# Kernel optimization log

Hardware: AMD Instinct MI355X
Metric: run time of the kernel (lower is better)

The kernel has to match this reference:

```python
import jax, jax.numpy as jnp
import numpy as np

EPS = 1e-5  # torch LayerNorm default


def setup_inputs() -> dict:
    key = jax.random.key(0)
    ks = jax.random.split(key, 4)
    B, S, D = 8, 1024, 768
    return {
        "q": jax.random.normal(ks[0], (B, S, D), dtype=jnp.float32),
        "k": jax.random.normal(ks[1], (B, S, D), dtype=jnp.float32),
        "v": jax.random.normal(ks[2], (B, S, D), dtype=jnp.float32),
        "W": jax.random.normal(ks[3], (D, D), dtype=jnp.float32) * (1.0 / np.sqrt(D)),
        "gamma": jnp.ones((D,), dtype=jnp.float32),
        "beta": jnp.zeros((D,), dtype=jnp.float32),
        "n_heads": 12,
    }


def reference(q, k, v, W, gamma, beta, n_heads):
    # Shapes: q,k,v [B,S,D]; W [D,D] (torch Linear weight, y = x @ W.T)
    B, S, D = q.shape
    Dh = D // n_heads

    proj = lambda x: jax.nn.relu(x @ W.T)
    q1, k1, v1 = proj(q), proj(k), proj(v)

    # chunk(dim=2) + cat(dim=0) == reshape to per-head [B,S,H,Dh]
    split = lambda x: x.reshape(B, S, n_heads, Dh)
    qh, kh, vh = split(q1), split(k1), split(v1)

    scale = 1.0 / (Dh ** 0.5)
    scores = jnp.einsum("bqhd,bkhd->bhqk", qh, kh) * scale  # [B,H,S,S]
    attn = jax.nn.softmax(scores, axis=-1)  # dropout is identity in eval mode
    out = jnp.einsum("bhqk,bkhd->bqhd", attn, vh).reshape(B, S, D)

    # `outputs += outputs + q` in torch -> outputs = 2*outputs + q
    out = 2.0 * out + q

    mu = jnp.mean(out, axis=-1, keepdims=True)
    var = jnp.var(out, axis=-1, keepdims=True)
    return (out - mu) / jnp.sqrt(var + EPS) * gamma + beta
```

## Files before the change

### kernel.cpp

```cpp
#include <hip/hip_runtime.h>
#include <hip/hip_bf16.h>

#define B_  8
#define S_  1024
#define D_  768
#define H_  12
#define DH_ 64

typedef __attribute__((ext_vector_type(8))) short bf16x8;
typedef __attribute__((ext_vector_type(4))) float f32x4;
typedef __attribute__((ext_vector_type(16))) float f32x16;

__device__ inline short f2bf(float f) {
    unsigned u = __builtin_bit_cast(unsigned, f);
    u = (u + 0x7fffu + ((u >> 16) & 1u)) >> 16;
    return (short)u;
}
__device__ inline float exp2_fast(float x) {
    float r; asm("v_exp_f32 %0, %1" : "=v"(r) : "v"(x)); return r;
}
__device__ inline unsigned cvt_pk_bf16(float lo, float hi) {
    unsigned r; asm("v_cvt_pk_bf16_f32 %0, %1, %2" : "=v"(r) : "v"(lo), "v"(hi)); return r;
}
__device__ inline float rcp_fast(float x) {
    float r; asm("v_rcp_f32 %0, %1" : "=v"(r) : "v"(x)); return r;
}
__device__ inline void plswap(unsigned& a, unsigned& b) {
    auto r = __builtin_amdgcn_permlane32_swap(a, b, false, false);
    a = r[0]; b = r[1];
}
__device__ inline float2 xhalves(float x) {
    unsigned u = __builtin_bit_cast(unsigned, x);
    auto r = __builtin_amdgcn_permlane32_swap(u, u, false, false);
    return make_float2(__builtin_bit_cast(float, r[0]),
                       __builtin_bit_cast(float, r[1]));
}
__device__ inline void gl_lds16(const float* gsrc, char* ldst) {
    __builtin_amdgcn_global_load_lds(
        (const __attribute__((address_space(1))) unsigned int*)gsrc,
        (__attribute__((address_space(3))) unsigned int*)ldst,
        16, 0, 0);
}

__global__ __launch_bounds__(256) void proj_kernel(
    const float* __restrict__ q, const float* __restrict__ k,
    const float* __restrict__ v, const float* __restrict__ W,
    short* __restrict__ q1, short* __restrict__ k1, short* __restrict__ v1t)
{
    __shared__ __align__(16) char lds_raw[32768];

    int p  = blockIdx.x;
    int L  = (p & 7) * 144 + (p >> 3);
    int mt = L / 6, nt = L % 6;
    int t  = mt >> 6;
    int m0 = (mt & 63) << 7;
    int n0 = nt << 7;
    const float* X = (t == 0) ? q : (t == 1) ? k : v;

    int tid = threadIdx.x, lane = tid & 63, w = tid >> 6;
    int wr = w >> 1, wc = w & 1;
    int l15 = lane & 15, g = lane >> 4;

    const float* srcA[4];
    const float* srcB[4];
    #pragma unroll
    for (int i = 0; i < 4; i++) {
        int r  = w * 32 + i * 8 + (lane >> 3);
        int sp = (lane & 7) ^ (r & 7);
        srcA[i] = X + (size_t)(m0 + r) * D_ + sp * 4;
        srcB[i] = W + (size_t)(n0 + r) * D_ + sp * 4;
    }

    f32x4 acc[4][4];
    #pragma unroll
    for (int m = 0; m < 4; m++)
        #pragma unroll
        for (int n = 0; n < 4; n++) acc[m][n] = (f32x4){0.f, 0.f, 0.f, 0.f};

    for (int kb = 0; kb < 24; ++kb) {
        __builtin_amdgcn_s_barrier();
        asm volatile("" ::: "memory");
        #pragma unroll
        for (int i = 0; i < 4; i++) {
            gl_lds16(srcA[i] + kb * 32, lds_raw + w * 4096 + i * 1024);
            gl_lds16(srcB[i] + kb * 32, lds_raw + 16384 + w * 4096 + i * 1024);
        }
        asm volatile("s_waitcnt vmcnt(0)" ::: "memory");
        __builtin_amdgcn_s_barrier();
        asm volatile("" ::: "memory");

        bf16x8 af[4], bfv[4];
        #pragma unroll
        for (int m = 0; m < 4; m++) {
            int r = wr * 64 + m * 16 + l15;
            const char* rp = lds_raw + r * 128;
            f32x4 lo = *(const f32x4*)(rp + (((2 * g)     ^ (r & 7)) << 4));
            f32x4 hi = *(const f32x4*)(rp + (((2 * g + 1) ^ (r & 7)) << 4));
            uint4 pk;
            pk.x = cvt_pk_bf16(lo[0], lo[1]); pk.y = cvt_pk_bf16(lo[2], lo[3]);
            pk.z = cvt_pk_bf16(hi[0], hi[1]); pk.w = cvt_pk_bf16(hi[2], hi[3]);
            af[m] = __builtin_bit_cast(bf16x8, pk);
        }
        #pragma unroll
        for (int n = 0; n < 4; n++) {
            int r = wc * 64 + n * 16 + l15;
            const char* rp = lds_raw + 16384 + r * 128;
            f32x4 lo = *(const f32x4*)(rp + (((2 * g)     ^ (r & 7)) << 4));
            f32x4 hi = *(const f32x4*)(rp + (((2 * g + 1) ^ (r & 7)) << 4));
            uint4 pk;
            pk.x = cvt_pk_bf16(lo[0], lo[1]); pk.y = cvt_pk_bf16(lo[2], lo[3]);
            pk.z = cvt_pk_bf16(hi[0], hi[1]); pk.w = cvt_pk_bf16(hi[2], hi[3]);
            bfv[n] = __builtin_bit_cast(bf16x8, pk);
        }
        __builtin_amdgcn_s_setprio(1);
        #pragma unroll
        for (int m = 0; m < 4; m++)
            #pragma unroll
            for (int n = 0; n < 4; n++)
                acc[m][n] = __builtin_amdgcn_mfma_f32_16x16x32_bf16(
                    af[m], bfv[n], acc[m][n], 0, 0, 0);
        __builtin_amdgcn_s_setprio(0);
    }

    __syncthreads();
    const float sc1 = (t == 1) ? 0.18033688011112793f : 1.0f;
    #pragma unroll
    for (int m = 0; m < 4; m++) {
        int rb = wr * 64 + m * 16 + (g << 2);
        #pragma unroll
        for (int n = 0; n < 4; n++) {
            int cb = wc * 64 + n * 16 + l15;
            #pragma unroll
            for (int r = 0; r < 4; r++) {
                short vv = f2bf(fmaxf(acc[m][n][r], 0.f) * sc1);
                int rr = (t == 2) ? cb : rb + r;
                int cc = (t == 2) ? rb + r : cb;
                *(short*)(lds_raw + rr * 256 + (((cc >> 3) ^ (rr & 15)) << 4)
                          + ((cc & 7) << 1)) = vv;
            }
        }
    }
    __syncthreads();
    int row = tid >> 1;
    int c0  = (tid & 1) << 6;
    bf16x8 ov[8];
    #pragma unroll
    for (int j = 0; j < 8; j++)
        ov[j] = *(const bf16x8*)(lds_raw + row * 256 +
                 ((((c0 >> 3) + j) ^ (row & 15)) << 4));
    if (t == 2) {
        int gc = n0 + row;
        int hh2 = gc >> 6, dh = gc & 63;
        int bb = m0 >> 10, s0 = m0 & 1023;
        short* dst = v1t + (((size_t)bb * H_ + hh2) * DH_ + dh) * S_ + s0 + c0;
        #pragma unroll
        for (int j = 0; j < 8; j++) *(bf16x8*)(dst + j * 8) = ov[j];
    } else {
        int m = m0 + row;
        int bb = m >> 10, ss = m & 1023;
        int hh2 = (n0 >> 6) + (tid & 1);
        short* dst = (t ? k1 : q1) + (((size_t)bb * H_ + hh2) * S_ + ss) * DH_;
        #pragma unroll
        for (int j = 0; j < 8; j++) *(bf16x8*)(dst + j * 8) = ov[j];
    }
}

__global__ __launch_bounds__(256, 3) void attn_kernel(
    const short* __restrict__ q1, const short* __restrict__ k1,
    const short* __restrict__ v1t, float* __restrict__ out)
{
    __shared__ short Klds[2][4096];
    __shared__ short Vlds[2][4096];
    __shared__ float lsum_lds[4][32];

    int d    = blockIdx.x;
    int head = (d & 7) + ((d >> 6) << 3);
    int qi   = (d >> 3) & 7;
    int bb   = head / H_, hh = head % H_;

    int tid = threadIdx.x, lane = tid & 63, w = tid >> 6;
    int l31 = lane & 31, hi = lane >> 5;
    int qbase = (qi * 4 + w) * 32;

    const short* Qp = q1  + (size_t)head * S_ * DH_;
    const short* Kp = k1  + (size_t)head * S_ * DH_;
    const short* Vp = v1t + (size_t)head * DH_ * S_;

    int sr = tid >> 2, sc = tid & 3;
    int swz0 = sr * 128 + ((sc       ^ (sr & 7)) << 4);
    int swz1 = sr * 128 + (((sc + 4) ^ (sr & 7)) << 4);

    bf16x8 stK0, stK1, stV0, stV1;

#define LOADST(kvb) do { \
        const short* _kg = Kp + (size_t)((kvb) + sr) * DH_; \
        const short* _vg = Vp + (size_t)sr * S_ + (kvb); \
        stK0 = *(const bf16x8*)(_kg + sc * 8); \
        stK1 = *(const bf16x8*)(_kg + (sc + 4) * 8); \
        stV0 = *(const bf16x8*)(_vg + sc * 8); \
        stV1 = *(const bf16x8*)(_vg + (sc + 4) * 8); \
    } while (0)
#define WRITEST(buf) do { \
        char* _kb = (char*)&Klds[buf][0]; \
        char* _vb = (char*)&Vlds[buf][0]; \
        *(bf16x8*)(_kb + swz0) = stK0; \
        *(bf16x8*)(_kb + swz1) = stK1; \
        *(bf16x8*)(_vb + swz0) = stV0; \
        *(bf16x8*)(_vb + swz1) = stV1; \
    } while (0)

    bf16x8 qf[4];
    #pragma unroll
    for (int kb = 0; kb < 4; kb++)
        qf[kb] = *(const bf16x8*)(Qp + (size_t)(qbase + l31) * DH_ + kb * 16 + hi * 8);

    f32x16 o0, o1;
    #pragma unroll
    for (int r = 0; r < 16; r++) { o0[r] = 0.f; o1[r] = 0.f; }
    float mreg = -1e30f, lsum = 0.f;

    int xk = l31 & 7;

    auto subtile = [&](int cur, int j) {
        const char* Kt = (const char*)&Klds[cur][0];
        const char* Vt = (const char*)&Vlds[cur][0];
        int rK = (32 * j + l31) * 128;
        bf16x8 kf0 = *(const bf16x8*)(Kt + rK + (((0 + hi) ^ xk) << 4));
        bf16x8 kf1 = *(const bf16x8*)(Kt + rK + (((2 + hi) ^ xk) << 4));
        bf16x8 kf2 = *(const bf16x8*)(Kt + rK + (((4 + hi) ^ xk) << 4));
        bf16x8 kf3 = *(const bf16x8*)(Kt + rK + (((6 + hi) ^ xk) << 4));
        int rV0 = l31 * 128, rV1 = (32 + l31) * 128;
        int s0 = ((4 * j + hi) ^ xk) << 4, s1 = ((4 * j + 2 + hi) ^ xk) << 4;
        bf16x8 vf00 = *(const bf16x8*)(Vt + rV0 + s0);
        bf16x8 vf01 = *(const bf16x8*)(Vt + rV0 + s1);
        bf16x8 vf10 = *(const bf16x8*)(Vt + rV1 + s0);
        bf16x8 vf11 = *(const bf16x8*)(Vt + rV1 + s1);

        f32x16 s;
        #pragma unroll
        for (int r = 0; r < 16; r++) s[r] = 0.f;
        __builtin_amdgcn_s_setprio(1);
        s = __builtin_amdgcn_mfma_f32_32x32x16_bf16(kf0, qf[0], s, 0, 0, 0);
        s = __builtin_amdgcn_mfma_f32_32x32x16_bf16(kf1, qf[1], s, 0, 0, 0);
        s = __builtin_amdgcn_mfma_f32_32x32x16_bf16(kf2, qf[2], s, 0, 0, 0);
        s = __builtin_amdgcn_mfma_f32_32x32x16_bf16(kf3, qf[3], s, 0, 0, 0);
        __builtin_amdgcn_s_setprio(0);

        float t0 = fmaxf(s[0], s[1]),   t1 = fmaxf(s[2], s[3]);
        float t2 = fmaxf(s[4], s[5]),   t3 = fmaxf(s[6], s[7]);
        float t4 = fmaxf(s[8], s[9]),   t5 = fmaxf(s[10], s[11]);
        float t6 = fmaxf(s[12], s[13]), t7 = fmaxf(s[14], s[15]);
        float u0 = fmaxf(t0, t1), u1 = fmaxf(t2, t3);
        float u2 = fmaxf(t4, t5), u3 = fmaxf(t6, t7);
        float pmax = fmaxf(fmaxf(u0, u1), fmaxf(u2, u3));
        float2 ph = xhalves(pmax);
        pmax = fmaxf(ph.x, ph.y);

        if (!__all(pmax <= mreg + 8.f)) {
            float mn = fmaxf(mreg, pmax);
            float sc_ = exp2_fast(mreg - mn);
            mreg = mn; lsum *= sc_;
            if (hi == 0) lsum_lds[w][l31] = sc_;
            asm volatile("s_waitcnt lgkmcnt(0)" ::: "memory");
            #pragma unroll
            for (int r = 0; r < 16; r++) {
                int crow = (r & 3) + ((r >> 2) << 3) + (hi << 2);
                float srw = lsum_lds[w][crow];
                o0[r] *= srw; o1[r] *= srw;
            }
        }

        #pragma unroll
        for (int r = 0; r < 16; r++) s[r] = exp2_fast(s[r] - mreg);

        float a0 = s[0] + s[1],   a1 = s[2] + s[3];
        float a2 = s[4] + s[5],   a3 = s[6] + s[7];
        float a4 = s[8] + s[9],   a5 = s[10] + s[11];
        float a6 = s[12] + s[13], a7 = s[14] + s[15];
        float rsum = ((a0 + a1) + (a2 + a3)) + ((a4 + a5) + (a6 + a7));
        float2 rh = xhalves(rsum);
        lsum += rh.x + rh.y;

        unsigned c0 = cvt_pk_bf16(s[0], s[1]);
        unsigned c1 = cvt_pk_bf16(s[2], s[3]);
        unsigned c2 = cvt_pk_bf16(s[4], s[5]);
        unsigned c3 = cvt_pk_bf16(s[6], s[7]);
        unsigned c4 = cvt_pk_bf16(s[8], s[9]);
        unsigned c5 = cvt_pk_bf16(s[10], s[11]);
        unsigned c6 = cvt_pk_bf16(s[12], s[13]);
        unsigned c7 = cvt_pk_bf16(s[14], s[15]);
        plswap(c0, c2);
        plswap(c1, c3);
        plswap(c4, c6);
        plswap(c5, c7);

        union U { unsigned u[4]; bf16x8 v; };
        U f0, f1;
        f0.u[0] = c0; f0.u[1] = c1; f0.u[2] = c2; f0.u[3] = c3;
        f1.u[0] = c4; f1.u[1] = c5; f1.u[2] = c6; f1.u[3] = c7;

        __builtin_amdgcn_s_setprio(1);
        o0 = __builtin_amdgcn_mfma_f32_32x32x16_bf16(f0.v, vf00, o0, 0, 0, 0);
        o0 = __builtin_amdgcn_mfma_f32_32x32x16_bf16(f1.v, vf01, o0, 0, 0, 0);
        o1 = __builtin_amdgcn_mfma_f32_32x32x16_bf16(f0.v, vf10, o1, 0, 0, 0);
        o1 = __builtin_amdgcn_mfma_f32_32x32x16_bf16(f1.v, vf11, o1, 0, 0, 0);
        __builtin_amdgcn_s_setprio(0);
    };

    LOADST(0);
    WRITEST(0);
    LOADST(64);
    asm volatile("s_waitcnt lgkmcnt(0)" ::: "memory");
    __builtin_amdgcn_s_barrier();
    asm volatile("" ::: "memory");

    int cur = 0;
    for (int t = 0; t < 16; t++) {
        if (t < 15) {
            WRITEST(cur ^ 1);
            if (t < 14) LOADST((t + 2) * 64);
        }
        subtile(cur, 0);
        subtile(cur, 1);
        if (t < 15) {
            asm volatile("" ::: "memory");
            asm volatile("s_waitcnt lgkmcnt(0)" ::: "memory");
            __builtin_amdgcn_s_barrier();
            asm volatile("" ::: "memory");
        }
        cur ^= 1;
    }
#undef LOADST
#undef WRITEST

    if (hi == 0) lsum_lds[w][l31] = lsum;
    asm volatile("s_waitcnt lgkmcnt(0)" ::: "memory");
    #pragma unroll
    for (int r = 0; r < 16; r++) {
        int crow = (r & 3) + ((r >> 2) << 3) + (hi << 2);
        float inv = rcp_fast(lsum_lds[w][crow]);
        float* op = out + ((size_t)(bb * S_ + qbase + crow)) * D_ + hh * DH_ + l31;
        op[0]  = o0[r] * inv;
        op[32] = o1[r] * inv;
    }
}

__global__ __launch_bounds__(192) void ln_kernel(
    const float* __restrict__ qin, const float* __restrict__ gamma,
    const float* __restrict__ beta, float* __restrict__ out)
{
    int row = blockIdx.x;
    int tid = threadIdx.x;
    size_t base = (size_t)row * D_ + tid * 4;

    f32x4 o  = *(const f32x4*)(out + base);
    f32x4 qv = *(const f32x4*)(qin + base);
    f32x4 x;
    float sum = 0.f, sq = 0.f;
    #pragma unroll
    for (int i = 0; i < 4; i++) {
        x[i] = 2.f * o[i] + qv[i];
        sum += x[i];
        sq  += x[i] * x[i];
    }
    #pragma unroll
    for (int msk = 1; msk < 64; msk <<= 1) {
        sum += __shfl_xor(sum, msk);
        sq  += __shfl_xor(sq, msk);
    }
    __shared__ float s1[3], s2[3];
    if ((tid & 63) == 0) { s1[tid >> 6] = sum; s2[tid >> 6] = sq; }
    __syncthreads();
    sum = s1[0] + s1[1] + s1[2];
    sq  = s2[0] + s2[1] + s2[2];
    float mu   = sum * (1.f / D_);
    float var  = sq * (1.f / D_) - mu * mu;
    float rstd = rsqrtf(var + 1e-5f);
    f32x4 g = *(const f32x4*)(gamma + tid * 4);
    f32x4 b = *(const f32x4*)(beta + tid * 4);
    f32x4 y;
    #pragma unroll
    for (int i = 0; i < 4; i++)
        y[i] = (x[i] - mu) * rstd * g[i] + b[i];
    *(f32x4*)(out + base) = y;
}

extern "C" void kernel_launch(void* const* d_in, const int* in_sizes, int n_in,
                              void* d_out, int out_size, void* d_ws, size_t ws_size,
                              hipStream_t stream)
{
    const float* q     = (const float*)d_in[0];
    const float* k     = (const float*)d_in[1];
    const float* v     = (const float*)d_in[2];
    const float* W     = (const float*)d_in[3];
    const float* gamma = (const float*)d_in[4];
    const float* beta  = (const float*)d_in[5];

    size_t per = (size_t)B_ * H_ * S_ * DH_;
    short* q1  = (short*)d_ws;
    short* k1  = q1 + per;
    short* v1t = k1 + per;
    float* out = (float*)d_out;

    proj_kernel<<<dim3(1152), dim3(256), 0, stream>>>(q, k, v, W, q1, k1, v1t);
    attn_kernel<<<dim3(768), dim3(256), 0, stream>>>(q1, k1, v1t, out);
    ln_kernel<<<dim3(B_ * S_), dim3(192), 0, stream>>>(q, gamma, beta, out);
}
```

Measured before the change: 128.0 us.

## Pre-convert W to bf16 and retile projection GEMM with double-buffered loads

Adds a small kernel that converts W to bf16 once per call, so the projection GEMM loads half the weight bytes and skips per-tile conversion of B operands. The projection kernel moves to 512 threads with 64x384 tiles, where each wave owns 48 output columns, and the LDS loads become double-buffered so the next k-slice is fetched during compute. The epilogue is rewritten for the new tile shape. The cost is an extra kernel launch, a larger LDS footprint (64KB) and a workspace buffer for Wb.

Result: faster. 117.5 us, median of 2 (-8.2%).

```diff
diff --git a/kernel.cpp b/kernel.cpp
--- a/kernel.cpp
+++ b/kernel.cpp
@@ -35,65 +35,86 @@
     return make_float2(__builtin_bit_cast(float, r[0]),
                        __builtin_bit_cast(float, r[1]));
 }
-__device__ inline void gl_lds16(const float* gsrc, char* ldst) {
+__device__ inline void gl_lds16(const void* gsrc, char* ldst) {
     __builtin_amdgcn_global_load_lds(
         (const __attribute__((address_space(1))) unsigned int*)gsrc,
         (__attribute__((address_space(3))) unsigned int*)ldst,
         16, 0, 0);
 }
 
-__global__ __launch_bounds__(256) void proj_kernel(
+__global__ __launch_bounds__(256) void convw_kernel(
+    const float* __restrict__ W, short* __restrict__ Wb)
+{
+    int i = (blockIdx.x * 256 + threadIdx.x) * 8;
+    f32x4 a = *(const f32x4*)(W + i);
+    f32x4 b = *(const f32x4*)(W + i + 4);
+    uint4 pk;
+    pk.x = cvt_pk_bf16(a[0], a[1]); pk.y = cvt_pk_bf16(a[2], a[3]);
+    pk.z = cvt_pk_bf16(b[0], b[1]); pk.w = cvt_pk_bf16(b[2], b[3]);
+    *(uint4*)(Wb + i) = pk;
+}
+
+__global__ __launch_bounds__(512) void proj_kernel(
     const float* __restrict__ q, const float* __restrict__ k,
-    const float* __restrict__ v, const float* __restrict__ W,
+    const float* __restrict__ v, const short* __restrict__ Wb,
     short* __restrict__ q1, short* __restrict__ k1, short* __restrict__ v1t)
 {
-    __shared__ __align__(16) char lds_raw[32768];
+    __shared__ __align__(16) char lds[65536];
 
     int p  = blockIdx.x;
-    int L  = (p & 7) * 144 + (p >> 3);
-    int mt = L / 6, nt = L % 6;
-    int t  = mt >> 6;
-    int m0 = (mt & 63) << 7;
-    int n0 = nt << 7;
+    int L  = (p & 7) * 96 + (p >> 3);
+    int mt = L >> 1, nb = L & 1;
+    int t  = mt >> 7;
+    int m0 = (mt & 127) << 6;
+    int n0 = nb * 384;
     const float* X = (t == 0) ? q : (t == 1) ? k : v;
 
     int tid = threadIdx.x, lane = tid & 63, w = tid >> 6;
-    int wr = w >> 1, wc = w & 1;
     int l15 = lane & 15, g = lane >> 4;
 
-    const float* srcA[4];
-    const float* srcB[4];
-    #pragma unroll
-    for (int i = 0; i < 4; i++) {
-        int r  = w * 32 + i * 8 + (lane >> 3);
-        int sp = (lane & 7) ^ (r & 7);
-        srcA[i] = X + (size_t)(m0 + r) * D_ + sp * 4;
-        srcB[i] = W + (size_t)(n0 + r) * D_ + sp * 4;
-    }
-
-    f32x4 acc[4][4];
+    int xrow = w * 8 + (lane >> 3), xc = lane & 7;
+    const float* xsrc = X + (size_t)(m0 + xrow) * D_ + ((xc ^ (xrow & 7)) << 2);
+    char* xdst = lds + w * 1024;
+    int wrow0 = w * 48 + (lane >> 2), wc = lane & 3;
+    int wrow1 = wrow0 + 16, wrow2 = wrow0 + 32;
+    const short* wsrc0 = Wb + (size_t)(n0 + wrow0) * D_ + ((wc ^ ((wrow0 >> 1) & 3)) << 3);
+    const short* wsrc1 = Wb + (size_t)(n0 + wrow1) * D_ + ((wc ^ ((wrow1 >> 1) & 3)) << 3);
+    const short* wsrc2 = Wb + (size_t)(n0 + wrow2) * D_ + ((wc ^ ((wrow2 >> 1) & 3)) << 3);
+    char* wdst = lds + 16384 + w * 3072;
+
+#define ISSUE(s_, b_) do { int _ko = (s_) * 32; \
+        gl_lds16(xsrc + _ko, xdst + (b_) * 8192); \
+        gl_lds16(wsrc0 + _ko, wdst + (b_) * 24576); \
+        gl_lds16(wsrc1 + _ko, wdst + (b_) * 24576 + 1024); \
+        gl_lds16(wsrc2 + _ko, wdst + (b_) * 24576 + 2048); \
+    } while (0)
+
+    f32x4 acc[4][3];
     #pragma unroll
     for (int m = 0; m < 4; m++)
         #pragma unroll
-        for (int n = 0; n < 4; n++) acc[m][n] = (f32x4){0.f, 0.f, 0.f, 0.f};
-
-    for (int kb = 0; kb < 24; ++kb) {
+        for (int n = 0; n < 3; n++) acc[m][n] = (f32x4){0.f, 0.f, 0.f, 0.f};
+
+    ISSUE(0, 0);
+    for (int s = 0; s < 24; ++s) {
         __builtin_amdgcn_s_barrier();
         asm volatile("" ::: "memory");
-        #pragma unroll
-        for (int i = 0; i < 4; i++) {
-            gl_lds16(srcA[i] + kb * 32, lds_raw + w * 4096 + i * 1024);
-            gl_lds16(srcB[i] + kb * 32, lds_raw + 16384 + w * 4096 + i * 1024);
-        }
-        asm volatile("s_waitcnt vmcnt(0)" ::: "memory");
+        if (s + 1 < 24) {
+            ISSUE(s + 1, (s + 1) & 1);
+            asm volatile("s_waitcnt vmcnt(4)" ::: "memory");
+        } else {
+            asm volatile("s_waitcnt vmcnt(0)" ::: "memory");
+        }
         __builtin_amdgcn_s_barrier();
         asm volatile("" ::: "memory");
 
-        bf16x8 af[4], bfv[4];
+        const char* Xb = lds + (s & 1) * 8192;
+        const char* Wp = lds + 16384 + (s & 1) * 24576;
+        bf16x8 af[4];
         #pragma unroll
         for (int m = 0; m < 4; m++) {
-            int r = wr * 64 + m * 16 + l15;
-            const char* rp = lds_raw + r * 128;
+            int r = m * 16 + l15;
+            const char* rp = Xb + r * 128;
             f32x4 lo = *(const f32x4*)(rp + (((2 * g)     ^ (r & 7)) << 4));
             f32x4 hi = *(const f32x4*)(rp + (((2 * g + 1) ^ (r & 7)) << 4));
             uint4 pk;
@@ -101,67 +122,64 @@
             pk.z = cvt_pk_bf16(hi[0], hi[1]); pk.w = cvt_pk_bf16(hi[2], hi[3]);
             af[m] = __builtin_bit_cast(bf16x8, pk);
         }
-        #pragma unroll
-        for (int n = 0; n < 4; n++) {
-            int r = wc * 64 + n * 16 + l15;
-            const char* rp = lds_raw + 16384 + r * 128;
-            f32x4 lo = *(const f32x4*)(rp + (((2 * g)     ^ (r & 7)) << 4));
-            f32x4 hi = *(const f32x4*)(rp + (((2 * g + 1) ^ (r & 7)) << 4));
-            uint4 pk;
-            pk.x = cvt_pk_bf16(lo[0], lo[1]); pk.y = cvt_pk_bf16(lo[2], lo[3]);
-            pk.z = cvt_pk_bf16(hi[0], hi[1]); pk.w = cvt_pk_bf16(hi[2], hi[3]);
-            bfv[n] = __builtin_bit_cast(bf16x8, pk);
+        bf16x8 bfv[3];
+        #pragma unroll
+        for (int n = 0; n < 3; n++) {
+            int r = w * 48 + n * 16 + l15;
+            bfv[n] = *(const bf16x8*)(Wp + r * 64 + ((g ^ ((r >> 1) & 3)) << 4));
         }
         __builtin_amdgcn_s_setprio(1);
         #pragma unroll
         for (int m = 0; m < 4; m++)
             #pragma unroll
-            for (int n = 0; n < 4; n++)
+            for (int n = 0; n < 3; n++)
                 acc[m][n] = __builtin_amdgcn_mfma_f32_16x16x32_bf16(
                     af[m], bfv[n], acc[m][n], 0, 0, 0);
         __builtin_amdgcn_s_setprio(0);
     }
+#undef ISSUE
 
     __syncthreads();
     const float sc1 = (t == 1) ? 0.18033688011112793f : 1.0f;
     #pragma unroll
-    for (int m = 0; m < 4; m++) {
-        int rb = wr * 64 + m * 16 + (g << 2);
-        #pragma unroll
-        for (int n = 0; n < 4; n++) {
-            int cb = wc * 64 + n * 16 + l15;
+    for (int m = 0; m < 4; m++)
+        #pragma unroll
+        for (int n = 0; n < 3; n++)
             #pragma unroll
             for (int r = 0; r < 4; r++) {
+                int row = m * 16 + g * 4 + r;
+                int col = w * 48 + n * 16 + l15;
                 short vv = f2bf(fmaxf(acc[m][n][r], 0.f) * sc1);
-                int rr = (t == 2) ? cb : rb + r;
-                int cc = (t == 2) ? rb + r : cb;
-                *(short*)(lds_raw + rr * 256 + (((cc >> 3) ^ (rr & 15)) << 4)
-                          + ((cc & 7) << 1)) = vv;
+                if (t == 2)
+                    *(short*)(lds + col * 128 + (((row >> 3) ^ (col & 7)) << 4)
+                              + ((row & 7) << 1)) = vv;
+                else
+                    *(short*)(lds + row * 768 + (((col >> 3) ^ (row & 7)) << 4)
+                              + ((col & 7) << 1)) = vv;
             }
-        }
-    }
     __syncthreads();
-    int row = tid >> 1;
-    int c0  = (tid & 1) << 6;
-    bf16x8 ov[8];
-    #pragma unroll
-    for (int j = 0; j < 8; j++)
-        ov[j] = *(const bf16x8*)(lds_raw + row * 256 +
-                 ((((c0 >> 3) + j) ^ (row & 15)) << 4));
+    int bb2 = m0 >> 10;
     if (t == 2) {
-        int gc = n0 + row;
-        int hh2 = gc >> 6, dh = gc & 63;
-        int bb = m0 >> 10, s0 = m0 & 1023;
-        short* dst = v1t + (((size_t)bb * H_ + hh2) * DH_ + dh) * S_ + s0 + c0;
-        #pragma unroll
-        for (int j = 0; j < 8; j++) *(bf16x8*)(dst + j * 8) = ov[j];
+        #pragma unroll
+        for (int j = 0; j < 6; j++) {
+            int c = tid * 6 + j;
+            int vr = c >> 3, ch = c & 7;
+            bf16x8 val = *(const bf16x8*)(lds + vr * 128 + ((ch ^ (vr & 7)) << 4));
+            int gc = n0 + vr, h = gc >> 6, dh = gc & 63;
+            *(bf16x8*)(v1t + (((size_t)bb2 * H_ + h) * DH_ + dh) * S_
+                       + (m0 & 1023) + ch * 8) = val;
+        }
     } else {
-        int m = m0 + row;
-        int bb = m >> 10, ss = m & 1023;
-        int hh2 = (n0 >> 6) + (tid & 1);
-        short* dst = (t ? k1 : q1) + (((size_t)bb * H_ + hh2) * S_ + ss) * DH_;
-        #pragma unroll
-        for (int j = 0; j < 8; j++) *(bf16x8*)(dst + j * 8) = ov[j];
+        short* dst0 = t ? k1 : q1;
+        #pragma unroll
+        for (int j = 0; j < 6; j++) {
+            int c = tid * 6 + j;
+            int row = c / 48, ch = c % 48;
+            bf16x8 val = *(const bf16x8*)(lds + row * 768 + ((ch ^ (row & 7)) << 4));
+            int m = m0 + row, ss = m & 1023;
+            int gc = n0 + ch * 8, h = gc >> 6, dh = gc & 63;
+            *(bf16x8*)(dst0 + (((size_t)bb2 * H_ + h) * S_ + ss) * DH_ + dh) = val;
+        }
     }
 }
 
@@ -400,9 +418,11 @@
     short* q1  = (short*)d_ws;
     short* k1  = q1 + per;
     short* v1t = k1 + per;
+    short* Wb  = v1t + per;
     float* out = (float*)d_out;
 
-    proj_kernel<<<dim3(1152), dim3(256), 0, stream>>>(q, k, v, W, q1, k1, v1t);
+    convw_kernel<<<dim3(288), dim3(256), 0, stream>>>(W, Wb);
+    proj_kernel<<<dim3(768), dim3(512), 0, stream>>>(q, k, v, Wb, q1, k1, v1t);
     attn_kernel<<<dim3(768), dim3(256), 0, stream>>>(q1, k1, v1t, out);
     ln_kernel<<<dim3(B_ * S_), dim3(192), 0, stream>>>(q, gamma, beta, out);
 }
```

## Pre-convert W to bf16 and register-prefetch activations in projection GEMM

Applied to the files above, without the earlier changes.

A new small kernel converts the weight matrix to bf16 once per call, so the projection kernel loads bf16 W tiles straight into LDS and no longer converts them on every tile read. Activation tiles are now prefetched into registers one K-step ahead, converted to bf16 and written to LDS, which overlaps global loads with MFMA work. The K step doubles to 64 with two MFMA sub-steps per barrier, halving the number of barriers. The cost is an extra kernel launch, more workspace, higher register pressure from the prefetch buffers, and reliance on the workspace being large enough for Wb.

Result: slower. 155.7 us (+21.6%).

```diff
diff --git a/kernel.cpp b/kernel.cpp
--- a/kernel.cpp
+++ b/kernel.cpp
@@ -35,19 +35,31 @@
     return make_float2(__builtin_bit_cast(float, r[0]),
                        __builtin_bit_cast(float, r[1]));
 }
-__device__ inline void gl_lds16(const float* gsrc, char* ldst) {
+__device__ inline void gl_lds16(const void* gsrc, char* ldst) {
     __builtin_amdgcn_global_load_lds(
         (const __attribute__((address_space(1))) unsigned int*)gsrc,
         (__attribute__((address_space(3))) unsigned int*)ldst,
         16, 0, 0);
 }
 
+__global__ __launch_bounds__(256) void convw_kernel(
+    const float* __restrict__ W, short* __restrict__ Wb)
+{
+    int i = (blockIdx.x * 256 + threadIdx.x) * 8;
+    f32x4 a = *(const f32x4*)(W + i);
+    f32x4 b = *(const f32x4*)(W + i + 4);
+    uint4 pk;
+    pk.x = cvt_pk_bf16(a[0], a[1]); pk.y = cvt_pk_bf16(a[2], a[3]);
+    pk.z = cvt_pk_bf16(b[0], b[1]); pk.w = cvt_pk_bf16(b[2], b[3]);
+    *(uint4*)(Wb + i) = pk;
+}
+
 __global__ __launch_bounds__(256) void proj_kernel(
     const float* __restrict__ q, const float* __restrict__ k,
-    const float* __restrict__ v, const float* __restrict__ W,
+    const float* __restrict__ v, const short* __restrict__ Wb,
     short* __restrict__ q1, short* __restrict__ k1, short* __restrict__ v1t)
 {
-    __shared__ __align__(16) char lds_raw[32768];
+    __shared__ __align__(16) char lds[32768];
 
     int p  = blockIdx.x;
     int L  = (p & 7) * 144 + (p >> 3);
@@ -61,15 +73,29 @@
     int wr = w >> 1, wc = w & 1;
     int l15 = lane & 15, g = lane >> 4;
 
-    const float* srcA[4];
-    const float* srcB[4];
+    const short* bsrc[4];
+    char*        bdst[4];
     #pragma unroll
     for (int i = 0; i < 4; i++) {
-        int r  = w * 32 + i * 8 + (lane >> 3);
-        int sp = (lane & 7) ^ (r & 7);
-        srcA[i] = X + (size_t)(m0 + r) * D_ + sp * 4;
-        srcB[i] = W + (size_t)(n0 + r) * D_ + sp * 4;
-    }
+        int r = w * 32 + i * 8 + (lane >> 3);
+        int c = lane & 7;
+        bsrc[i] = Wb + (size_t)(n0 + r) * D_ + ((c ^ (r & 7)) << 3);
+        bdst[i] = lds + 16384 + w * 4096 + i * 1024;
+    }
+
+    int tr = tid >> 1, ch = tid & 1;
+    const float* asrc = X + (size_t)(m0 + tr) * D_ + ch * 32;
+    int awb[4];
+    #pragma unroll
+    for (int j = 0; j < 4; j++)
+        awb[j] = tr * 128 + (((4 * ch + j) ^ (tr & 7)) << 4);
+
+    f32x4 pf[8];
+#define LOADA(s_) do { \
+        _Pragma("unroll") \
+        for (int j = 0; j < 8; j++) \
+            pf[j] = *(const f32x4*)(asrc + (s_) * 64 + j * 4); \
+    } while (0)
 
     f32x4 acc[4][4];
     #pragma unroll
@@ -77,50 +103,57 @@
         #pragma unroll
         for (int n = 0; n < 4; n++) acc[m][n] = (f32x4){0.f, 0.f, 0.f, 0.f};
 
-    for (int kb = 0; kb < 24; ++kb) {
+    LOADA(0);
+    for (int s = 0; s < 12; ++s) {
         __builtin_amdgcn_s_barrier();
         asm volatile("" ::: "memory");
         #pragma unroll
-        for (int i = 0; i < 4; i++) {
-            gl_lds16(srcA[i] + kb * 32, lds_raw + w * 4096 + i * 1024);
-            gl_lds16(srcB[i] + kb * 32, lds_raw + 16384 + w * 4096 + i * 1024);
-        }
-        asm volatile("s_waitcnt vmcnt(0)" ::: "memory");
+        for (int i = 0; i < 4; i++)
+            gl_lds16(bsrc[i] + s * 64, bdst[i]);
+        #pragma unroll
+        for (int j = 0; j < 4; j++) {
+            uint4 u;
+            u.x = cvt_pk_bf16(pf[2 * j][0], pf[2 * j][1]);
+            u.y = cvt_pk_bf16(pf[2 * j][2], pf[2 * j][3]);
+            u.z = cvt_pk_bf16(pf[2 * j + 1][0], pf[2 * j + 1][1]);
+            u.w = cvt_pk_bf16(pf[2 * j + 1][2], pf[2 * j + 1][3]);
+            *(uint4*)(lds + awb[j]) = u;
+        }
+        if (s + 1 < 12) {
+            LOADA(s + 1);
+            asm volatile("s_waitcnt vmcnt(8) lgkmcnt(0)" ::: "memory");
+        } else {
+            asm volatile("s_waitcnt vmcnt(0) lgkmcnt(0)" ::: "memory");
+        }
         __builtin_amdgcn_s_barrier();
         asm volatile("" ::: "memory");
 
-        bf16x8 af[4], bfv[4];
-        #pragma unroll
-        for (int m = 0; m < 4; m++) {
-            int r = wr * 64 + m * 16 + l15;
-            const char* rp = lds_raw + r * 128;
-            f32x4 lo = *(const f32x4*)(rp + (((2 * g)     ^ (r & 7)) << 4));
-            f32x4 hi = *(const f32x4*)(rp + (((2 * g + 1) ^ (r & 7)) << 4));
-            uint4 pk;
-            pk.x = cvt_pk_bf16(lo[0], lo[1]); pk.y = cvt_pk_bf16(lo[2], lo[3]);
-            pk.z = cvt_pk_bf16(hi[0], hi[1]); pk.w = cvt_pk_bf16(hi[2], hi[3]);
-            af[m] = __builtin_bit_cast(bf16x8, pk);
-        }
-        #pragma unroll
-        for (int n = 0; n < 4; n++) {
-            int r = wc * 64 + n * 16 + l15;
-            const char* rp = lds_raw + 16384 + r * 128;
-            f32x4 lo = *(const f32x4*)(rp + (((2 * g)     ^ (r & 7)) << 4));
-            f32x4 hi = *(const f32x4*)(rp + (((2 * g + 1) ^ (r & 7)) << 4));
-            uint4 pk;
-            pk.x = cvt_pk_bf16(lo[0], lo[1]); pk.y = cvt_pk_bf16(lo[2], lo[3]);
-            pk.z = cvt_pk_bf16(hi[0], hi[1]); pk.w = cvt_pk_bf16(hi[2], hi[3]);
-            bfv[n] = __builtin_bit_cast(bf16x8, pk);
-        }
-        __builtin_amdgcn_s_setprio(1);
-        #pragma unroll
-        for (int m = 0; m < 4; m++)
+        #pragma unroll
+        for (int kk = 0; kk < 2; kk++) {
+            bf16x8 af[4], bfv[4];
             #pragma unroll
-            for (int n = 0; n < 4; n++)
-                acc[m][n] = __builtin_amdgcn_mfma_f32_16x16x32_bf16(
-                    af[m], bfv[n], acc[m][n], 0, 0, 0);
-        __builtin_amdgcn_s_setprio(0);
-    }
+            for (int m = 0; m < 4; m++) {
+                int ra = wr * 64 + m * 16 + l15;
+                af[m] = *(const bf16x8*)(lds + ra * 128 +
+                         ((((kk << 2) | g) ^ (ra & 7)) << 4));
+            }
+            #pragma unroll
+            for (int n = 0; n < 4; n++) {
+                int rb = wc * 64 + n * 16 + l15;
+                bfv[n] = *(const bf16x8*)(lds + 16384 + rb * 128 +
+                          ((((kk << 2) | g) ^ (rb & 7)) << 4));
+            }
+            __builtin_amdgcn_s_setprio(1);
+            #pragma unroll
+            for (int m = 0; m < 4; m++)
+                #pragma unroll
+                for (int n = 0; n < 4; n++)
+                    acc[m][n] = __builtin_amdgcn_mfma_f32_16x16x32_bf16(
+                        af[m], bfv[n], acc[m][n], 0, 0, 0);
+            __builtin_amdgcn_s_setprio(0);
+        }
+    }
+#undef LOADA
 
     __syncthreads();
     const float sc1 = (t == 1) ? 0.18033688011112793f : 1.0f;
@@ -135,7 +168,7 @@
                 short vv = f2bf(fmaxf(acc[m][n][r], 0.f) * sc1);
                 int rr = (t == 2) ? cb : rb + r;
                 int cc = (t == 2) ? rb + r : cb;
-                *(short*)(lds_raw + rr * 256 + (((cc >> 3) ^ (rr & 15)) << 4)
+                *(short*)(lds + rr * 256 + (((cc >> 3) ^ (rr & 15)) << 4)
                           + ((cc & 7) << 1)) = vv;
             }
         }
@@ -146,7 +179,7 @@
     bf16x8 ov[8];
     #pragma unroll
     for (int j = 0; j < 8; j++)
-        ov[j] = *(const bf16x8*)(lds_raw + row * 256 +
+        ov[j] = *(const bf16x8*)(lds + row * 256 +
                  ((((c0 >> 3) + j) ^ (row & 15)) << 4));
     if (t == 2) {
         int gc = n0 + row;
@@ -400,9 +433,11 @@
     short* q1  = (short*)d_ws;
     short* k1  = q1 + per;
     short* v1t = k1 + per;
+    short* Wb  = v1t + per;
     float* out = (float*)d_out;
 
-    proj_kernel<<<dim3(1152), dim3(256), 0, stream>>>(q, k, v, W, q1, k1, v1t);
+    convw_kernel<<<dim3(288), dim3(256), 0, stream>>>(W, Wb);
+    proj_kernel<<<dim3(1152), dim3(256), 0, stream>>>(q, k, v, Wb, q1, k1, v1t);
     attn_kernel<<<dim3(768), dim3(256), 0, stream>>>(q1, k1, v1t, out);
     ln_kernel<<<dim3(B_ * S_), dim3(192), 0, stream>>>(q, gamma, beta, out);
 }
```
